# Kernel tuning notes

Hardware: AMD Instinct MI355X
Metric: run time of the kernel (lower is better)

## Reference

```python
import jax, jax.numpy as jnp
import numpy as np

N, N2, N3 = 40000, 20000, 10000
E, E2, E3 = 640000, 320000, 160000
HEADS = 4
F_IN = 5


def _glorot(k, shape):
    lim = float(np.sqrt(6.0 / (shape[0] + shape[-1])))
    return jax.random.uniform(k, shape, jnp.float32, -lim, lim)


def setup_inputs() -> dict:
    key = jax.random.key(0)
    ks = jax.random.split(key, 40)
    inp = {}
    inp["x"] = jax.random.normal(ks[0], (N, F_IN), jnp.float32)
    inp["edge_index"] = jax.random.randint(ks[1], (2, E), 0, N)
    inp["edge_index2"] = jax.random.randint(ks[2], (2, E2), 0, N2)
    inp["edge_index3"] = jax.random.randint(ks[3], (2, E3), 0, N3)
    # graclus-style cluster maps; constructed surjective so no cluster is empty
    inp["cluster1"] = jax.random.permutation(ks[4], jnp.arange(N) % N2)
    inp["cluster2"] = jax.random.permutation(ks[5], jnp.arange(N2) % N3)
    dims = [(F_IN, 16), (16, 32), (32, 64), (64, 32), (64, 16)]
    i = 6
    for idx, (fi, fo) in enumerate(dims, 1):
        inp[f"cW{idx}"] = _glorot(ks[i], (fi, HEADS * fo)); i += 1
        inp[f"cU{idx}"] = _glorot(ks[i], (fi, HEADS)); i += 1
        inp[f"cc{idx}"] = jnp.zeros((HEADS,), jnp.float32)
        inp[f"cb{idx}"] = jnp.zeros((fo,), jnp.float32)
    inp["l1W"] = _glorot(ks[i], (32, 256)); i += 1
    inp["l1b"] = jnp.zeros((256,), jnp.float32)
    inp["l2W"] = _glorot(ks[i], (256, 6890)); i += 1
    inp["l2b"] = jnp.zeros((6890,), jnp.float32)
    inp["oW"] = _glorot(ks[i], (6890, 1)); i += 1
    inp["ob"] = jnp.zeros((1,), jnp.float32)
    return inp


def feast_conv(x, ei, W, U, c, b, n, fo):
    """PyG FeaStConv: self-loops, per-edge head-softmax attention, mean aggregation."""
    sl = jnp.arange(n)
    src = jnp.concatenate([ei[0], sl])  # message sources (x_j)
    dst = jnp.concatenate([ei[1], sl])  # aggregation targets (x_i)
    xs, xd = x[src], x[dst]
    q = jax.nn.softmax((xs - xd) @ U + c, axis=-1)          # [E+n, H]
    m = (xs @ W).reshape(-1, HEADS, fo)                      # [E+n, H, fo]
    msg = jnp.einsum('eh,eho->eo', q, m)                     # [E+n, fo]
    agg = jax.ops.segment_sum(msg, dst, num_segments=n)
    cnt = jax.ops.segment_sum(jnp.ones((dst.shape[0],), x.dtype), dst, num_segments=n)
    return agg / cnt[:, None] + b


def _forward(x, edge_index, edge_index2, edge_index3, cluster1, cluster2, p):
    x1 = jax.nn.relu(feast_conv(x, edge_index, p["cW1"], p["cU1"], p["cc1"], p["cb1"], N, 16))
    x2 = jax.ops.segment_max(x1, cluster1, num_segments=N2)                     # graclus max_pool
    x2 = jax.nn.relu(feast_conv(x2, edge_index2, p["cW2"], p["cU2"], p["cc2"], p["cb2"], N2, 32))
    x3 = jax.ops.segment_max(x2, cluster2, num_segments=N3)
    x3 = jax.nn.relu(feast_conv(x3, edge_index3, p["cW3"], p["cU3"], p["cc3"], p["cb3"], N3, 64))
    x3 = jax.nn.relu(feast_conv(x3, edge_index3, p["cW4"], p["cU4"], p["cc4"], p["cb4"], N3, 32))
    x3 = jnp.concatenate([x2, x3[cluster2]], axis=1)                            # [N2, 64] unpool+skip
    x3 = jax.nn.relu(feast_conv(x3, edge_index2, p["cW5"], p["cU5"], p["cc5"], p["cb5"], N2, 16))
    h = jnp.concatenate([x1, x3[cluster1]], axis=1)                             # [N, 32]
    h = jax.nn.relu(h @ p["l1W"] + p["l1b"])
    h = jax.nn.relu(h @ p["l2W"] + p["l2b"])                                   # [N, 6890]
    return jax.nn.sigmoid(h @ p["oW"] + p["ob"])                                # [N, 1]


def reference(x, edge_index, edge_index2, edge_index3, cluster1, cluster2,
              cW1, cU1, cc1, cb1, cW2, cU2, cc2, cb2, cW3, cU3, cc3, cb3,
              cW4, cU4, cc4, cb4, cW5, cU5, cc5, cb5, l1W, l1b, l2W, l2b, oW, ob):
    p = dict(cW1=cW1, cU1=cU1, cc1=cc1, cb1=cb1, cW2=cW2, cU2=cU2, cc2=cc2, cb2=cb2,
             cW3=cW3, cU3=cU3, cc3=cc3, cb3=cb3, cW4=cW4, cU4=cU4, cc4=cc4, cb4=cb4,
             cW5=cW5, cU5=cU5, cc5=cc5, cb5=cb5, l1W=l1W, l1b=l1b, l2W=l2W, l2b=l2b,
             oW=oW, ob=ob)
    return _forward(x, edge_index, edge_index2, edge_index3, cluster1, cluster2, p)
```

## Files before the change

### kernel.cpp

```cpp
#include <hip/hip_runtime.h>
#include <math.h>

#define N1  40000
#define NN2 20000
#define NN3 10000
#define EE1 640000
#define EE2 320000
#define EE3 160000
#define ET  (EE1 + EE2 + EE3)
#define JPAD 6912
#define JREAL 6890
#define NTILE 432
#define CSPLIT 8
#define TPB (NTILE/CSPLIT)
#define NSTG (TPB/2)
#define NROWP 40192
#define NGRP 628
#define CAP 64

typedef __attribute__((ext_vector_type(8))) short short8;
typedef __attribute__((ext_vector_type(4))) float f32x4;

__device__ inline unsigned short f2bf(float f) {
  unsigned u = __float_as_uint(f);
  u += 0x7FFF + ((u >> 16) & 1);
  return (unsigned short)(u >> 16);
}

__device__ inline f32x4 qsoft(f32x4 xs, f32x4 xd, float c0, float c1, float c2, float c3) {
  float l0 = xs[0] - xd[0] + c0, l1 = xs[1] - xd[1] + c1;
  float l2 = xs[2] - xd[2] + c2, l3 = xs[3] - xd[3] + c3;
  float mx = fmaxf(fmaxf(l0, l1), fmaxf(l2, l3));
  float q0 = __expf(l0 - mx), q1 = __expf(l1 - mx);
  float q2 = __expf(l2 - mx), q3 = __expf(l3 - mx);
  float iv = 1.f / (q0 + q1 + q2 + q3);
  return (f32x4){q0 * iv, q1 * iv, q2 * iv, q3 * iv};
}

__global__ void k_matmulWU(const float* __restrict__ Xa, int fa,
                           const float* __restrict__ Xb, int fb,
                           const int* __restrict__ map,
                           const float* __restrict__ W, const float* __restrict__ U,
                           float* __restrict__ xW, float* __restrict__ xU,
                           int n, int co) {
  int ct = co + 4;
  int idx = blockIdx.x * 256 + threadIdx.x;
  if (idx >= n * ct) return;
  int row = idx / ct, col = idx - row * ct;
  const float* M;
  int stride;
  if (col < co) { M = W + col; stride = co; }
  else          { M = U + (col - co); stride = 4; }
  float s = 0.f;
  const float* ar = Xa + (size_t)row * fa;
  for (int k = 0; k < fa; ++k) s = fmaf(ar[k], M[(size_t)k * stride], s);
  if (Xb) {
    const float* br = Xb + (size_t)map[row] * fb;
    for (int k = 0; k < fb; ++k) s = fmaf(br[k], M[(size_t)(fa + k) * stride], s);
  }
  if (col < co) xW[(size_t)row * co + col] = s;
  else          xU[(size_t)row * 4 + (col - co)] = s;
}

__global__ void k_xU(const float* __restrict__ xin, const float* __restrict__ U,
                     float* __restrict__ xu, int n, int ci) {
  int idx = blockIdx.x * 256 + threadIdx.x;
  if (idx >= n * 4) return;
  int h = idx & 3, d = idx >> 2;
  const float* xr = xin + (size_t)d * ci;
  float s = 0.f;
  for (int k = 0; k < ci; ++k) s = fmaf(xr[k], U[k * 4 + h], s);
  xu[idx] = s;
}

__global__ void k_prep(const int* __restrict__ ei1, const int* __restrict__ ei2,
                       const int* __restrict__ ei3,
                       int* __restrict__ c1, int* __restrict__ c2, int* __restrict__ c3,
                       int* __restrict__ s1, int* __restrict__ s2, int* __restrict__ s3,
                       const float* __restrict__ x, float* __restrict__ x8,
                       const float* __restrict__ U1, float* __restrict__ xu1) {
  int i = blockIdx.x * 256 + threadIdx.x;
  if (i < ET) {
    int e = i;
    const int* ei; int* cnt; int* sl; int E;
    if (e < EE1) { ei = ei1; cnt = c1; sl = s1; E = EE1; }
    else {
      e -= EE1;
      if (e < EE2) { ei = ei2; cnt = c2; sl = s2; E = EE2; }
      else { e -= EE2; ei = ei3; cnt = c3; sl = s3; E = EE3; }
    }
    int s = ei[e], d = ei[E + e];
    int pos = atomicAdd(&cnt[d], 1);
    if (pos < CAP) sl[(size_t)d * CAP + pos] = s;
    return;
  }
  i -= ET;
  if (i < N1 * 8) {
    int d = i >> 3, k = i & 7;
    x8[i] = (k < 5) ? x[d * 5 + k] : 0.f;
    return;
  }
  i -= N1 * 8;
  if (i < N1 * 4) {
    int h = i & 3, d = i >> 2;
    const float* xr = x + (size_t)d * 5;
    float s = 0.f;
#pragma unroll
    for (int k = 0; k < 5; ++k) s = fmaf(xr[k], U1[k * 4 + h], s);
    xu1[i] = s;
  }
}

template<int CI4, int FO, int KREAL>
__global__ __launch_bounds__(256) void k_aggf(
    const int* __restrict__ cnt, const int* __restrict__ slots,
    const float* __restrict__ xU, const f32x4* __restrict__ xin4, int stride4,
    const float* __restrict__ c, const float* __restrict__ W,
    const float* __restrict__ b, float* __restrict__ outp, int n,
    const int* __restrict__ pool_cl, int* __restrict__ pool_out) {
  constexpr int LPN = CI4 * 4;
  constexpr int NB  = 256 / LPN;
  __shared__ float sh[NB][CI4 * 16];
  const int tid = threadIdx.x;
  const int nl = tid / LPN, li = tid - nl * LPN;
  const int cg = li >> 2, sp = li & 3;
  const int d = blockIdx.x * NB + nl;
  const float c0 = c[0], c1 = c[1], c2 = c[2], c3 = c[3];
  const f32x4* XU4 = (const f32x4*)xU;

  if (d < n) {
    const f32x4 xd = XU4[d];
    const int deg = min(cnt[d], CAP);
    const int jlo = (deg * sp) >> 2, jhi = (deg * (sp + 1)) >> 2;
    const int* sl = slots + (size_t)d * CAP;
    f32x4 acc[4];
#pragma unroll
    for (int e = 0; e < 4; ++e) acc[e] = (f32x4){0.f, 0.f, 0.f, 0.f};
    int j = jlo;
    for (; j + 4 <= jhi; j += 4) {
      int s0 = sl[j], s1 = sl[j + 1], s2 = sl[j + 2], s3 = sl[j + 3];
      f32x4 u0 = XU4[s0], u1 = XU4[s1], u2 = XU4[s2], u3 = XU4[s3];
      f32x4 v0 = xin4[(size_t)s0 * stride4 + cg];
      f32x4 v1 = xin4[(size_t)s1 * stride4 + cg];
      f32x4 v2 = xin4[(size_t)s2 * stride4 + cg];
      f32x4 v3 = xin4[(size_t)s3 * stride4 + cg];
      f32x4 q0 = qsoft(u0, xd, c0, c1, c2, c3);
      f32x4 q1 = qsoft(u1, xd, c0, c1, c2, c3);
      f32x4 q2 = qsoft(u2, xd, c0, c1, c2, c3);
      f32x4 q3 = qsoft(u3, xd, c0, c1, c2, c3);
#pragma unroll
      for (int e = 0; e < 4; ++e)
        acc[e] += v0[e] * q0 + v1[e] * q1 + v2[e] * q2 + v3[e] * q3;
    }
    for (; j < jhi; ++j) {
      int s = sl[j];
      f32x4 u = XU4[s];
      f32x4 v = xin4[(size_t)s * stride4 + cg];
      f32x4 q = qsoft(u, xd, c0, c1, c2, c3);
#pragma unroll
      for (int e = 0; e < 4; ++e) acc[e] += v[e] * q;
    }
#pragma unroll
    for (int e = 0; e < 4; ++e)
#pragma unroll
      for (int h = 0; h < 4; ++h) {
        acc[e][h] += __shfl_xor(acc[e][h], 1);
        acc[e][h] += __shfl_xor(acc[e][h], 2);
      }
    if (sp == 0) {
      float mx = fmaxf(fmaxf(c0, c1), fmaxf(c2, c3));
      float q0 = __expf(c0 - mx), q1 = __expf(c1 - mx);
      float q2 = __expf(c2 - mx), q3 = __expf(c3 - mx);
      float iv = 1.f / (q0 + q1 + q2 + q3);
      f32x4 q = (f32x4){q0 * iv, q1 * iv, q2 * iv, q3 * iv};
      f32x4 xv = xin4[(size_t)d * stride4 + cg];
#pragma unroll
      for (int e = 0; e < 4; ++e) {
        f32x4 a = acc[e] + xv[e] * q;
#pragma unroll
        for (int h = 0; h < 4; ++h) sh[nl][(cg * 4 + e) * 4 + h] = a[h];
      }
    }
  }
  __syncthreads();

  constexpr int NBFO = NB * FO;
#pragma unroll
  for (int base = 0; base < NBFO; base += 256) {
    int i2 = base + tid;
    if (i2 < NBFO) {
      int ln = i2 / FO, o = i2 - ln * FO;
      int d2 = blockIdx.x * NB + ln;
      if (d2 < n) {
        float acc2 = 0.f;
        const float* shl = sh[ln];
        for (int k = 0; k < KREAL; ++k) {
          const float* wr = W + (size_t)k * (4 * FO) + o;
          acc2 += shl[k * 4 + 0] * wr[0] + shl[k * 4 + 1] * wr[FO]
                + shl[k * 4 + 2] * wr[2 * FO] + shl[k * 4 + 3] * wr[3 * FO];
        }
        int deg2 = min(cnt[d2], CAP);
        float v = fmaxf(acc2 / (float)(deg2 + 1) + b[o], 0.f);
        outp[(size_t)d2 * FO + o] = v;
        if (pool_cl)
          atomicMax((int*)&pool_out[(size_t)pool_cl[d2] * FO + o], __float_as_int(v));
      }
    }
  }
}

__global__ void k_attagg4(const int* __restrict__ cnt, const int* __restrict__ slots,
                          const float* __restrict__ xU, const float4* __restrict__ xW,
                          const float* __restrict__ c, const float4* __restrict__ b4,
                          float4* __restrict__ outp, int n, int fo4,
                          const int* __restrict__ pool_cl, int* __restrict__ pool_out) {
  int idx = blockIdx.x * 256 + threadIdx.x;
  if (idx >= n * fo4 * 4) return;
  const int sp = idx & 3;
  const int t = idx >> 2;
  const int d = t / fo4, og = t - d * fo4;
  const float c0 = c[0], c1 = c[1], c2 = c[2], c3 = c[3];
  const float4 xd = *(const float4*)&xU[(size_t)d * 4];
  const int deg = min(cnt[d], CAP);
  const int jlo = (deg * sp) >> 2;
  const int jhi = (deg * (sp + 1)) >> 2;
  const int* sl = slots + (size_t)d * CAP;
  float ax = 0.f, ay = 0.f, az = 0.f, aw = 0.f;
  int j = jlo;
  for (; j + 2 <= jhi; j += 2) {
    int sA = sl[j], sB = sl[j + 1];
    float4 xsA = *(const float4*)&xU[(size_t)sA * 4];
    float4 xsB = *(const float4*)&xU[(size_t)sB * 4];
    const float4* mA = xW + (size_t)sA * 4 * fo4 + og;
    const float4* mB = xW + (size_t)sB * 4 * fo4 + og;
    float4 a0 = mA[0], a1 = mA[fo4], a2 = mA[2 * fo4], a3 = mA[3 * fo4];
    float4 e0 = mB[0], e1 = mB[fo4], e2 = mB[2 * fo4], e3 = mB[3 * fo4];
    float lA0 = xsA.x - xd.x + c0, lA1 = xsA.y - xd.y + c1;
    float lA2 = xsA.z - xd.z + c2, lA3 = xsA.w - xd.w + c3;
    float mxA = fmaxf(fmaxf(lA0, lA1), fmaxf(lA2, lA3));
    float qA0 = __expf(lA0 - mxA), qA1 = __expf(lA1 - mxA);
    float qA2 = __expf(lA2 - mxA), qA3 = __expf(lA3 - mxA);
    float ivA = 1.f / (qA0 + qA1 + qA2 + qA3);
    qA0 *= ivA; qA1 *= ivA; qA2 *= ivA; qA3 *= ivA;
    float lB0 = xsB.x - xd.x + c0, lB1 = xsB.y - xd.y + c1;
    float lB2 = xsB.z - xd.z + c2, lB3 = xsB.w - xd.w + c3;
    float mxB = fmaxf(fmaxf(lB0, lB1), fmaxf(lB2, lB3));
    float qB0 = __expf(lB0 - mxB), qB1 = __expf(lB1 - mxB);
    float qB2 = __expf(lB2 - mxB), qB3 = __expf(lB3 - mxB);
    float ivB = 1.f / (qB0 + qB1 + qB2 + qB3);
    qB0 *= ivB; qB1 *= ivB; qB2 *= ivB; qB3 *= ivB;
    ax += qA0 * a0.x + qA1 * a1.x + qA2 * a2.x + qA3 * a3.x
        + qB0 * e0.x + qB1 * e1.x + qB2 * e2.x + qB3 * e3.x;
    ay += qA0 * a0.y + qA1 * a1.y + qA2 * a2.y + qA3 * a3.y
        + qB0 * e0.y + qB1 * e1.y + qB2 * e2.y + qB3 * e3.y;
    az += qA0 * a0.z + qA1 * a1.z + qA2 * a2.z + qA3 * a3.z
        + qB0 * e0.z + qB1 * e1.z + qB2 * e2.z + qB3 * e3.z;
    aw += qA0 * a0.w + qA1 * a1.w + qA2 * a2.w + qA3 * a3.w
        + qB0 * e0.w + qB1 * e1.w + qB2 * e2.w + qB3 * e3.w;
  }
  if (j < jhi) {
    int s = sl[j];
    float4 xs = *(const float4*)&xU[(size_t)s * 4];
    const float4* m = xW + (size_t)s * 4 * fo4 + og;
    float4 m0 = m[0], m1 = m[fo4], m2 = m[2 * fo4], m3 = m[3 * fo4];
    float l0 = xs.x - xd.x + c0, l1 = xs.y - xd.y + c1;
    float l2 = xs.z - xd.z + c2, l3 = xs.w - xd.w + c3;
    float mx = fmaxf(fmaxf(l0, l1), fmaxf(l2, l3));
    float q0 = __expf(l0 - mx), q1 = __expf(l1 - mx);
    float q2 = __expf(l2 - mx), q3 = __expf(l3 - mx);
    float inv = 1.f / (q0 + q1 + q2 + q3);
    q0 *= inv; q1 *= inv; q2 *= inv; q3 *= inv;
    ax += q0 * m0.x + q1 * m1.x + q2 * m2.x + q3 * m3.x;
    ay += q0 * m0.y + q1 * m1.y + q2 * m2.y + q3 * m3.y;
    az += q0 * m0.z + q1 * m1.z + q2 * m2.z + q3 * m3.z;
    aw += q0 * m0.w + q1 * m1.w + q2 * m2.w + q3 * m3.w;
  }
  ax += __shfl_xor(ax, 1); ay += __shfl_xor(ay, 1);
  az += __shfl_xor(az, 1); aw += __shfl_xor(aw, 1);
  ax += __shfl_xor(ax, 2); ay += __shfl_xor(ay, 2);
  az += __shfl_xor(az, 2); aw += __shfl_xor(aw, 2);
  if (sp) return;
  {
    float mx = fmaxf(fmaxf(c0, c1), fmaxf(c2, c3));
    float q0 = __expf(c0 - mx), q1 = __expf(c1 - mx);
    float q2 = __expf(c2 - mx), q3 = __expf(c3 - mx);
    float inv = 1.f / (q0 + q1 + q2 + q3);
    const float4* m = xW + (size_t)d * 4 * fo4 + og;
    float4 m0 = m[0], m1 = m[fo4], m2 = m[2 * fo4], m3 = m[3 * fo4];
    ax += (q0 * m0.x + q1 * m1.x + q2 * m2.x + q3 * m3.x) * inv;
    ay += (q0 * m0.y + q1 * m1.y + q2 * m2.y + q3 * m3.y) * inv;
    az += (q0 * m0.z + q1 * m1.z + q2 * m2.z + q3 * m3.z) * inv;
    aw += (q0 * m0.w + q1 * m1.w + q2 * m2.w + q3 * m3.w) * inv;
  }
  const float inv = 1.f / (float)(deg + 1);
  const float4 bb = b4[og];
  float4 v;
  v.x = fmaxf(ax * inv + bb.x, 0.f);
  v.y = fmaxf(ay * inv + bb.y, 0.f);
  v.z = fmaxf(az * inv + bb.z, 0.f);
  v.w = fmaxf(aw * inv + bb.w, 0.f);
  outp[(size_t)d * fo4 + og] = v;
  if (pool_cl) {
    int* po = pool_out + ((size_t)pool_cl[d] * fo4 + og) * 4;
    atomicMax(&po[0], __float_as_int(v.x));
    atomicMax(&po[1], __float_as_int(v.y));
    atomicMax(&po[2], __float_as_int(v.z));
    atomicMax(&po[3], __float_as_int(v.w));
  }
}

__global__ __launch_bounds__(256) void k_packB(
    const float* __restrict__ l2W, short8* __restrict__ Bp,
    const float* __restrict__ l2b, const float* __restrict__ oW,
    float* __restrict__ l2bp, float* __restrict__ oWp) {
  __shared__ float tile[32][65];
  const int bid = blockIdx.x, tid = threadIdx.x;
  if (bid < 27) {
    int j = bid * 256 + tid;
    l2bp[j] = (j < JREAL) ? l2b[j] : 0.f;
    oWp[j]  = (j < JREAL) ? oW[j]  : 0.f;
  }
  const int kg = bid / 108, jg = bid - kg * 108;
  const int k0 = kg * 32, j0 = jg * 64;
  const int kr = tid >> 6, jc = tid & 63;
  const int j = j0 + jc;
#pragma unroll
  for (int i = 0; i < 8; ++i) {
    int row = kr * 8 + i;
    tile[row][jc] = (j < JREAL) ? l2W[(size_t)(k0 + row) * JREAL + j] : 0.f;
  }
  __syncthreads();
  const int tt = tid >> 6, lane = tid & 63;
  short8 v;
#pragma unroll
  for (int i = 0; i < 8; ++i)
    v[i] = (short)f2bf(tile[((lane >> 4) << 3) + i][tt * 16 + (lane & 15)]);
  Bp[((size_t)(jg * 4 + tt) * 8 + kg) * 64 + lane] = v;
}

__global__ __launch_bounds__(256) void k_packh(
    const float* __restrict__ x1, const float* __restrict__ x5,
    const int* __restrict__ cl1, const float* __restrict__ l1W,
    const float* __restrict__ l1b, short8* __restrict__ Apack) {
  __shared__ float h1s[64][256];
  const int tid = threadIdx.x;
  const int row0 = blockIdx.x * 64;

  float wcol[32];
#pragma unroll
  for (int k = 0; k < 32; ++k) wcol[k] = l1W[k * 256 + tid];
  const float bt = l1b[tid];

  for (int r = 0; r < 64; ++r) {
    const int row = row0 + r;
    float s = bt;
    if (row < N1) {
      const float* a = x1 + (size_t)row * 16;
      const float* b = x5 + (size_t)cl1[row] * 16;
#pragma unroll
      for (int k = 0; k < 16; ++k) s = fmaf(a[k], wcol[k], s);
#pragma unroll
      for (int k = 0; k < 16; ++k) s = fmaf(b[k], wcol[16 + k], s);
    }
    h1s[r][tid ^ ((r & 7) << 3)] = fmaxf(s, 0.f);
  }
  __syncthreads();

#pragma unroll
  for (int j = 0; j < 8; ++j) {
    int s = j * 256 + tid;
    int l = s & 63, ks = (s >> 6) & 7, rb = s >> 9;
    int row = rb * 16 + (l & 15);
    int col0 = (ks * 32 + ((l >> 4) << 3)) ^ ((row & 7) << 3);
    const float* sp = &h1s[row][col0];
    short8 v;
#pragma unroll
    for (int i = 0; i < 8; ++i) v[i] = (short)f2bf(sp[i]);
    Apack[(size_t)blockIdx.x * 2048 + s] = v;
  }
}

__global__ __launch_bounds__(256, 2) void k_final2(
    const short8* __restrict__ Apack, const short8* __restrict__ Bp,
    const float* __restrict__ l2bp, const float* __restrict__ oWp,
    float* __restrict__ zbuf) {
  __shared__ short8 bufs[2][1024];
  const int tid = threadIdx.x, wid = tid >> 6, l = tid & 63;
  const int rg = blockIdx.x >> 3, cg = blockIdx.x & 7;
  const int lm = l & 15, lh = l >> 4;

  short8 af[4][8];
  {
    const short8* ap = Apack + (size_t)(rg * 4 + wid) * 2048 + l;
#pragma unroll
    for (int rb = 0; rb < 4; ++rb)
#pragma unroll
      for (int ks = 0; ks < 8; ++ks) af[rb][ks] = ap[rb * 512 + ks * 64];
  }

  const short8* bsrc = Bp + (size_t)cg * TPB * 512;
  short8 n0 = bsrc[tid], n1 = bsrc[256 + tid], n2 = bsrc[512 + tid], n3 = bsrc[768 + tid];
  bufs[0][tid] = n0; bufs[0][256 + tid] = n1;
  bufs[0][512 + tid] = n2; bufs[0][768 + tid] = n3;
  {
    const short8* p = bsrc + 1024;
    n0 = p[tid]; n1 = p[256 + tid]; n2 = p[512 + tid]; n3 = p[768 + tid];
  }
  asm volatile("s_waitcnt lgkmcnt(0)" ::: "memory");
  __builtin_amdgcn_s_barrier();
  asm volatile("" ::: "memory");

  float zp[4][4];
#pragma unroll
  for (int rb = 0; rb < 4; ++rb)
#pragma unroll
    for (int r = 0; r < 4; ++r) zp[rb][r] = 0.f;

  for (int st = 0; st < NSTG; ++st) {
    const int cur = st & 1;
    if (st + 1 < NSTG) {
      bufs[cur ^ 1][tid] = n0; bufs[cur ^ 1][256 + tid] = n1;
      bufs[cur ^ 1][512 + tid] = n2; bufs[cur ^ 1][768 + tid] = n3;
    }
    if (st + 2 < NSTG) {
      const short8* p = bsrc + (st + 2) * 1024;
      n0 = p[tid]; n1 = p[256 + tid]; n2 = p[512 + tid]; n3 = p[768 + tid];
    }
#pragma unroll
    for (int half = 0; half < 2; ++half) {
      short8 bfr[8];
#pragma unroll
      for (int ks = 0; ks < 8; ++ks) bfr[ks] = bufs[cur][half * 512 + ks * 64 + l];

      f32x4 acc[4];
#pragma unroll
      for (int rb = 0; rb < 4; ++rb) acc[rb] = (f32x4){0.f, 0.f, 0.f, 0.f};
      __builtin_amdgcn_s_setprio(1);
#pragma unroll
      for (int ks = 0; ks < 8; ++ks)
#pragma unroll
        for (int rb = 0; rb < 4; ++rb)
          acc[rb] = __builtin_amdgcn_mfma_f32_16x16x32_bf16(af[rb][ks], bfr[ks], acc[rb], 0, 0, 0);
      __builtin_amdgcn_s_setprio(0);

      const int j = (cg * TPB + st * 2 + half) * 16 + lm;
      const float lb = l2bp[j];
      const float ow = oWp[j];
#pragma unroll
      for (int rb = 0; rb < 4; ++rb)
#pragma unroll
        for (int r = 0; r < 4; ++r)
          zp[rb][r] += fmaxf(acc[rb][r] + lb, 0.f) * ow;
    }
    asm volatile("s_waitcnt lgkmcnt(0)" ::: "memory");
    __builtin_amdgcn_s_barrier();
    asm volatile("" ::: "memory");
  }

#pragma unroll
  for (int m = 1; m < 16; m <<= 1)
#pragma unroll
    for (int rb = 0; rb < 4; ++rb)
#pragma unroll
      for (int r = 0; r < 4; ++r)
        zp[rb][r] += __shfl_xor(zp[rb][r], m);

  if (lm == 0) {
    const int rbase = rg * 256 + wid * 64 + lh * 4;
#pragma unroll
    for (int rb = 0; rb < 4; ++rb)
#pragma unroll
      for (int r = 0; r < 4; ++r)
        atomicAdd(&zbuf[rbase + rb * 16 + r], zp[rb][r]);
  }
}

__global__ void k_sigm(const float* __restrict__ zbuf, const float* __restrict__ ob,
                       float* __restrict__ out) {
  int i = blockIdx.x * 256 + threadIdx.x;
  if (i >= N1) return;
  out[i] = 1.f / (1.f + expf(-(zbuf[i] + ob[0])));
}

static void run_conv(const float* xa, int fa, const float* xb, int fb, const int* gmap,
                     const int* cnt, const int* slots, int n, int fo,
                     const float* W, const float* U, const float* c, const float* b,
                     float* outp, float* xW, float* xU,
                     const int* pool_cl, int* pool_out, hipStream_t stream) {
  int co = 4 * fo;
  k_matmulWU<<<(n * (co + 4) + 255) / 256, 256, 0, stream>>>(xa, fa, xb, fb, gmap,
                                                             W, U, xW, xU, n, co);
  k_attagg4<<<(n * (fo / 4) * 4 + 255) / 256, 256, 0, stream>>>(
      cnt, slots, xU, (const float4*)xW, c, (const float4*)b, (float4*)outp, n, fo / 4,
      pool_cl, pool_out);
}

extern "C" void kernel_launch(void* const* d_in, const int* in_sizes, int n_in,
                              void* d_out, int out_size, void* d_ws, size_t ws_size,
                              hipStream_t stream) {
  const float* x   = (const float*)d_in[0];
  const int* ei1   = (const int*)d_in[1];
  const int* ei2   = (const int*)d_in[2];
  const int* ei3   = (const int*)d_in[3];
  const int* cl1   = (const int*)d_in[4];
  const int* cl2   = (const int*)d_in[5];
  const float* cW1 = (const float*)d_in[6],  *cU1 = (const float*)d_in[7],
             * cc1 = (const float*)d_in[8],  *cb1 = (const float*)d_in[9];
  const float* cW2 = (const float*)d_in[10], *cU2 = (const float*)d_in[11],
             * cc2 = (const float*)d_in[12], *cb2 = (const float*)d_in[13];
  const float* cW3 = (const float*)d_in[14], *cU3 = (const float*)d_in[15],
             * cc3 = (const float*)d_in[16], *cb3 = (const float*)d_in[17];
  const float* cW4 = (const float*)d_in[18], *cU4 = (const float*)d_in[19],
             * cc4 = (const float*)d_in[20], *cb4 = (const float*)d_in[21];
  const float* cW5 = (const float*)d_in[22], *cU5 = (const float*)d_in[23],
             * cc5 = (const float*)d_in[24], *cb5 = (const float*)d_in[25];
  const float* l1W = (const float*)d_in[26], *l1b = (const float*)d_in[27];
  const float* l2W = (const float*)d_in[28], *l2b = (const float*)d_in[29];
  const float* oW  = (const float*)d_in[30], *ob  = (const float*)d_in[31];

  float* ws = (float*)d_ws;
  float* x2p  = ws + 0;
  float* x3p  = ws + 320000;
  float* zbuf = ws + 640000;
  int*  cnt1  = (int*)(ws + 680192);
  int*  cnt2  = (int*)(ws + 720192);
  int*  cnt3  = (int*)(ws + 740192);
  int*  sl1   = (int*)(ws + 750192);
  int*  sl2   = (int*)(ws + 3310192);
  int*  sl3   = (int*)(ws + 4590192);
  float* x3a  = ws + 5230192;
  float* x3b  = ws + 5870192;
  float* x1   = ws + 6190192;
  float* x2   = ws + 6830192;
  float* x5   = ws + 7470192;
  short8* Bp  = (short8*)(ws + 7790192);
  float* l2bp = ws + 8674928;
  float* oWp  = ws + 8681840;
  float* xW   = ws + 8688752;
  float* xu   = ws + 11248752;
  float* x8   = ws + 11408752;
  short8* Apack = (short8*)(ws + 750192);

  hipMemsetAsync(ws, 0, 750192 * sizeof(float), stream);
  k_packB<<<864, 256, 0, stream>>>(l2W, Bp, l2b, oW, l2bp, oWp);

  k_prep<<<(ET + N1 * 8 + N1 * 4 + 255) / 256, 256, 0, stream>>>(
      ei1, ei2, ei3, cnt1, cnt2, cnt3, sl1, sl2, sl3, x, x8, cU1, xu);

  k_aggf<2, 16, 5><<<(N1 + 31) / 32, 256, 0, stream>>>(
      cnt1, sl1, xu, (const f32x4*)x8, 2, cc1, cW1, cb1, x1, N1, cl1, (int*)x2p);
  k_xU<<<(NN2 * 4 + 255) / 256, 256, 0, stream>>>(x2p, cU2, xu, NN2, 16);
  k_aggf<4, 32, 16><<<(NN2 + 15) / 16, 256, 0, stream>>>(
      cnt2, sl2, xu, (const f32x4*)x2p, 4, cc2, cW2, cb2, x2, NN2, cl2, (int*)x3p);
  k_xU<<<(NN3 * 4 + 255) / 256, 256, 0, stream>>>(x3p, cU3, xu, NN3, 32);
  k_aggf<8, 64, 32><<<(NN3 + 7) / 8, 256, 0, stream>>>(
      cnt3, sl3, xu, (const f32x4*)x3p, 8, cc3, cW3, cb3, x3a, NN3, nullptr, nullptr);
  k_xU<<<(NN3 * 4 + 255) / 256, 256, 0, stream>>>(x3a, cU4, xu, NN3, 64);
  k_aggf<16, 32, 64><<<(NN3 + 3) / 4, 256, 0, stream>>>(
      cnt3, sl3, xu, (const f32x4*)x3a, 16, cc4, cW4, cb4, x3b, NN3, nullptr, nullptr);
  run_conv(x2, 32, x3b, 32, cl2, cnt2, sl2, NN2, 16,
           cW5, cU5, cc5, cb5, x5, xW, xu, nullptr, nullptr, stream);

  k_packh<<<NGRP, 256, 0, stream>>>(x1, x5, cl1, l1W, l1b, Apack);
  k_final2<<<(NROWP / 256) * CSPLIT, 256, 0, stream>>>(Apack, Bp, l2bp, oWp, zbuf);
  k_sigm<<<(N1 + 255) / 256, 256, 0, stream>>>(zbuf, ob, (float*)d_out);
}
```

Before: 426.3 us.

## Merge weight packing into prep kernel, fuse next-layer xU, use 16-bit slots

The l2W bf16 packing kernel is merged into the edge-bucketing prep kernel as extra blocks, which saves one launch and lets the two independent jobs run concurrently. Layer 3's aggregation kernel now computes the next layer's x@U projection from shared memory, removing a separate k_xU launch. Neighbor slot arrays are stored as 16-bit indices to halve slot traffic, which assumes node ids fit in 16 bits. With N1=40000 ids below 65536 this holds, but the code would break for larger graphs.

```diff
diff --git a/kernel.cpp b/kernel.cpp
--- a/kernel.cpp
+++ b/kernel.cpp
@@ -17,9 +17,11 @@
 #define NROWP 40192
 #define NGRP 628
 #define CAP 64
+#define PBK 864
 
 typedef __attribute__((ext_vector_type(8))) short short8;
 typedef __attribute__((ext_vector_type(4))) float f32x4;
+typedef unsigned short u16;
 
 __device__ inline unsigned short f2bf(float f) {
   unsigned u = __float_as_uint(f);
@@ -73,16 +75,46 @@
   xu[idx] = s;
 }
 
-__global__ void k_prep(const int* __restrict__ ei1, const int* __restrict__ ei2,
-                       const int* __restrict__ ei3,
-                       int* __restrict__ c1, int* __restrict__ c2, int* __restrict__ c3,
-                       int* __restrict__ s1, int* __restrict__ s2, int* __restrict__ s3,
-                       const float* __restrict__ x, float* __restrict__ x8,
-                       const float* __restrict__ U1, float* __restrict__ xu1) {
-  int i = blockIdx.x * 256 + threadIdx.x;
+__global__ __launch_bounds__(256) void k_setup(
+    const float* __restrict__ l2W, short8* __restrict__ Bp,
+    const float* __restrict__ l2b, const float* __restrict__ oW,
+    float* __restrict__ l2bp, float* __restrict__ oWp,
+    const int* __restrict__ ei1, const int* __restrict__ ei2,
+    const int* __restrict__ ei3,
+    int* __restrict__ c1, int* __restrict__ c2, int* __restrict__ c3,
+    u16* __restrict__ s1, u16* __restrict__ s2, u16* __restrict__ s3,
+    const float* __restrict__ x, float* __restrict__ x8,
+    const float* __restrict__ U1, float* __restrict__ xu1) {
+  __shared__ float tile[32][65];
+  const int bid = blockIdx.x, tid = threadIdx.x;
+  if (bid < PBK) {
+    if (bid < 27) {
+      int j = bid * 256 + tid;
+      l2bp[j] = (j < JREAL) ? l2b[j] : 0.f;
+      oWp[j]  = (j < JREAL) ? oW[j]  : 0.f;
+    }
+    const int kg = bid / 108, jg = bid - kg * 108;
+    const int k0 = kg * 32, j0 = jg * 64;
+    const int kr = tid >> 6, jc = tid & 63;
+    const int j = j0 + jc;
+#pragma unroll
+    for (int i = 0; i < 8; ++i) {
+      int row = kr * 8 + i;
+      tile[row][jc] = (j < JREAL) ? l2W[(size_t)(k0 + row) * JREAL + j] : 0.f;
+    }
+    __syncthreads();
+    const int tt = tid >> 6, lane = tid & 63;
+    short8 v;
+#pragma unroll
+    for (int i = 0; i < 8; ++i)
+      v[i] = (short)f2bf(tile[((lane >> 4) << 3) + i][tt * 16 + (lane & 15)]);
+    Bp[((size_t)(jg * 4 + tt) * 8 + kg) * 64 + lane] = v;
+    return;
+  }
+  int i = (bid - PBK) * 256 + tid;
   if (i < ET) {
     int e = i;
-    const int* ei; int* cnt; int* sl; int E;
+    const int* ei; int* cnt; u16* sl; int E;
     if (e < EE1) { ei = ei1; cnt = c1; sl = s1; E = EE1; }
     else {
       e -= EE1;
@@ -91,7 +123,7 @@
     }
     int s = ei[e], d = ei[E + e];
     int pos = atomicAdd(&cnt[d], 1);
-    if (pos < CAP) sl[(size_t)d * CAP + pos] = s;
+    if (pos < CAP) sl[(size_t)d * CAP + pos] = (u16)s;
     return;
   }
   i -= ET;
@@ -111,16 +143,18 @@
   }
 }
 
-template<int CI4, int FO, int KREAL>
+template<int CI4, int FO, int KREAL, bool XUOUT>
 __global__ __launch_bounds__(256) void k_aggf(
-    const int* __restrict__ cnt, const int* __restrict__ slots,
+    const int* __restrict__ cnt, const u16* __restrict__ slots,
     const float* __restrict__ xU, const f32x4* __restrict__ xin4, int stride4,
     const float* __restrict__ c, const float* __restrict__ W,
     const float* __restrict__ b, float* __restrict__ outp, int n,
-    const int* __restrict__ pool_cl, int* __restrict__ pool_out) {
+    const int* __restrict__ pool_cl, int* __restrict__ pool_out,
+    const float* __restrict__ Unext, float* __restrict__ xunext) {
   constexpr int LPN = CI4 * 4;
   constexpr int NB  = 256 / LPN;
   __shared__ float sh[NB][CI4 * 16];
+  __shared__ float sh2[NB][FO];
   const int tid = threadIdx.x;
   const int nl = tid / LPN, li = tid - nl * LPN;
   const int cg = li >> 2, sp = li & 3;
@@ -132,7 +166,7 @@
     const f32x4 xd = XU4[d];
     const int deg = min(cnt[d], CAP);
     const int jlo = (deg * sp) >> 2, jhi = (deg * (sp + 1)) >> 2;
-    const int* sl = slots + (size_t)d * CAP;
+    const u16* sl = slots + (size_t)d * CAP;
     f32x4 acc[4];
 #pragma unroll
     for (int e = 0; e < 4; ++e) acc[e] = (f32x4){0.f, 0.f, 0.f, 0.f};
@@ -202,14 +236,29 @@
         int deg2 = min(cnt[d2], CAP);
         float v = fmaxf(acc2 / (float)(deg2 + 1) + b[o], 0.f);
         outp[(size_t)d2 * FO + o] = v;
+        if (XUOUT) sh2[ln][o] = v;
         if (pool_cl)
           atomicMax((int*)&pool_out[(size_t)pool_cl[d2] * FO + o], __float_as_int(v));
       }
     }
   }
-}
-
-__global__ void k_attagg4(const int* __restrict__ cnt, const int* __restrict__ slots,
+
+  if (XUOUT) {
+    __syncthreads();
+    if (tid < NB * 4) {
+      int ln = tid >> 2, h = tid & 3;
+      int d3 = blockIdx.x * NB + ln;
+      if (d3 < n) {
+        float s = 0.f;
+        const float* so = sh2[ln];
+        for (int o = 0; o < FO; ++o) s = fmaf(so[o], Unext[o * 4 + h], s);
+        xunext[(size_t)d3 * 4 + h] = s;
+      }
+    }
+  }
+}
+
+__global__ void k_attagg4(const int* __restrict__ cnt, const u16* __restrict__ slots,
                           const float* __restrict__ xU, const float4* __restrict__ xW,
                           const float* __restrict__ c, const float4* __restrict__ b4,
                           float4* __restrict__ outp, int n, int fo4,
@@ -224,7 +273,7 @@
   const int deg = min(cnt[d], CAP);
   const int jlo = (deg * sp) >> 2;
   const int jhi = (deg * (sp + 1)) >> 2;
-  const int* sl = slots + (size_t)d * CAP;
+  const u16* sl = slots + (size_t)d * CAP;
   float ax = 0.f, ay = 0.f, az = 0.f, aw = 0.f;
   int j = jlo;
   for (; j + 2 <= jhi; j += 2) {
@@ -309,35 +358,6 @@
   }
 }
 
-__global__ __launch_bounds__(256) void k_packB(
-    const float* __restrict__ l2W, short8* __restrict__ Bp,
-    const float* __restrict__ l2b, const float* __restrict__ oW,
-    float* __restrict__ l2bp, float* __restrict__ oWp) {
-  __shared__ float tile[32][65];
-  const int bid = blockIdx.x, tid = threadIdx.x;
-  if (bid < 27) {
-    int j = bid * 256 + tid;
-    l2bp[j] = (j < JREAL) ? l2b[j] : 0.f;
-    oWp[j]  = (j < JREAL) ? oW[j]  : 0.f;
-  }
-  const int kg = bid / 108, jg = bid - kg * 108;
-  const int k0 = kg * 32, j0 = jg * 64;
-  const int kr = tid >> 6, jc = tid & 63;
-  const int j = j0 + jc;
-#pragma unroll
-  for (int i = 0; i < 8; ++i) {
-    int row = kr * 8 + i;
-    tile[row][jc] = (j < JREAL) ? l2W[(size_t)(k0 + row) * JREAL + j] : 0.f;
-  }
-  __syncthreads();
-  const int tt = tid >> 6, lane = tid & 63;
-  short8 v;
-#pragma unroll
-  for (int i = 0; i < 8; ++i)
-    v[i] = (short)f2bf(tile[((lane >> 4) << 3) + i][tt * 16 + (lane & 15)]);
-  Bp[((size_t)(jg * 4 + tt) * 8 + kg) * 64 + lane] = v;
-}
-
 __global__ __launch_bounds__(256) void k_packh(
     const float* __restrict__ x1, const float* __restrict__ x5,
     const int* __restrict__ cl1, const float* __restrict__ l1W,
@@ -480,19 +500,6 @@
   int i = blockIdx.x * 256 + threadIdx.x;
   if (i >= N1) return;
   out[i] = 1.f / (1.f + expf(-(zbuf[i] + ob[0])));
-}
-
-static void run_conv(const float* xa, int fa, const float* xb, int fb, const int* gmap,
-                     const int* cnt, const int* slots, int n, int fo,
-                     const float* W, const float* U, const float* c, const float* b,
-                     float* outp, float* xW, float* xU,
-                     const int* pool_cl, int* pool_out, hipStream_t stream) {
-  int co = 4 * fo;
-  k_matmulWU<<<(n * (co + 4) + 255) / 256, 256, 0, stream>>>(xa, fa, xb, fb, gmap,
-                                                             W, U, xW, xU, n, co);
-  k_attagg4<<<(n * (fo / 4) * 4 + 255) / 256, 256, 0, stream>>>(
-      cnt, slots, xU, (const float4*)xW, c, (const float4*)b, (float4*)outp, n, fo / 4,
-      pool_cl, pool_out);
 }
 
 extern "C" void kernel_launch(void* const* d_in, const int* in_sizes, int n_in,
@@ -525,41 +532,49 @@
   int*  cnt1  = (int*)(ws + 680192);
   int*  cnt2  = (int*)(ws + 720192);
   int*  cnt3  = (int*)(ws + 740192);
-  int*  sl1   = (int*)(ws + 750192);
-  int*  sl2   = (int*)(ws + 3310192);
-  int*  sl3   = (int*)(ws + 4590192);
-  float* x3a  = ws + 5230192;
-  float* x3b  = ws + 5870192;
-  float* x1   = ws + 6190192;
-  float* x2   = ws + 6830192;
-  float* x5   = ws + 7470192;
-  short8* Bp  = (short8*)(ws + 7790192);
-  float* l2bp = ws + 8674928;
-  float* oWp  = ws + 8681840;
-  float* xW   = ws + 8688752;
-  float* xu   = ws + 11248752;
-  float* x8   = ws + 11408752;
-  short8* Apack = (short8*)(ws + 750192);
+  float* x1   = ws + 750192;
+  float* x2   = ws + 1390192;
+  float* x5   = ws + 2030192;
+  short8* Bp  = (short8*)(ws + 2350192);
+  float* l2bp = ws + 3234928;
+  float* oWp  = ws + 3241840;
+  u16*  sl1   = (u16*)(ws + 3248752);
+  u16*  sl2   = (u16*)(ws + 4528752);
+  u16*  sl3   = (u16*)(ws + 5168752);
+  float* x3a  = ws + 5488752;
+  float* x3b  = ws + 6128752;
+  float* x8   = ws + 6448752;
+  float* xu   = ws + 6768752;
+  float* xub  = ws + 6928752;
+  float* xW   = ws + 6968752;
+  short8* Apack = (short8*)(ws + 3248752);
 
   hipMemsetAsync(ws, 0, 750192 * sizeof(float), stream);
-  k_packB<<<864, 256, 0, stream>>>(l2W, Bp, l2b, oW, l2bp, oWp);
-
-  k_prep<<<(ET + N1 * 8 + N1 * 4 + 255) / 256, 256, 0, stream>>>(
+
+  const int prepThreads = ET + N1 * 8 + N1 * 4;
+  k_setup<<<PBK + (prepThreads + 255) / 256, 256, 0, stream>>>(
+      l2W, Bp, l2b, oW, l2bp, oWp,
       ei1, ei2, ei3, cnt1, cnt2, cnt3, sl1, sl2, sl3, x, x8, cU1, xu);
 
-  k_aggf<2, 16, 5><<<(N1 + 31) / 32, 256, 0, stream>>>(
-      cnt1, sl1, xu, (const f32x4*)x8, 2, cc1, cW1, cb1, x1, N1, cl1, (int*)x2p);
+  k_aggf<2, 16, 5, false><<<(N1 + 31) / 32, 256, 0, stream>>>(
+      cnt1, sl1, xu, (const f32x4*)x8, 2, cc1, cW1, cb1, x1, N1, cl1, (int*)x2p,
+      nullptr, nullptr);
   k_xU<<<(NN2 * 4 + 255) / 256, 256, 0, stream>>>(x2p, cU2, xu, NN2, 16);
-  k_aggf<4, 32, 16><<<(NN2 + 15) / 16, 256, 0, stream>>>(
-      cnt2, sl2, xu, (const f32x4*)x2p, 4, cc2, cW2, cb2, x2, NN2, cl2, (int*)x3p);
+  k_aggf<4, 32, 16, false><<<(NN2 + 15) / 16, 256, 0, stream>>>(
+      cnt2, sl2, xu, (const f32x4*)x2p, 4, cc2, cW2, cb2, x2, NN2, cl2, (int*)x3p,
+      nullptr, nullptr);
   k_xU<<<(NN3 * 4 + 255) / 256, 256, 0, stream>>>(x3p, cU3, xu, NN3, 32);
-  k_aggf<8, 64, 32><<<(NN3 + 7) / 8, 256, 0, stream>>>(
-      cnt3, sl3, xu, (const f32x4*)x3p, 8, cc3, cW3, cb3, x3a, NN3, nullptr, nullptr);
-  k_xU<<<(NN3 * 4 + 255) / 256, 256, 0, stream>>>(x3a, cU4, xu, NN3, 64);
-  k_aggf<16, 32, 64><<<(NN3 + 3) / 4, 256, 0, stream>>>(
-      cnt3, sl3, xu, (const f32x4*)x3a, 16, cc4, cW4, cb4, x3b, NN3, nullptr, nullptr);
-  run_conv(x2, 32, x3b, 32, cl2, cnt2, sl2, NN2, 16,
-           cW5, cU5, cc5, cb5, x5, xW, xu, nullptr, nullptr, stream);
+  k_aggf<8, 64, 32, true><<<(NN3 + 7) / 8, 256, 0, stream>>>(
+      cnt3, sl3, xu, (const f32x4*)x3p, 8, cc3, cW3, cb3, x3a, NN3, nullptr, nullptr,
+      cU4, xub);
+  k_aggf<16, 32, 64, false><<<(NN3 + 3) / 4, 256, 0, stream>>>(
+      cnt3, sl3, xub, (const f32x4*)x3a, 16, cc4, cW4, cb4, x3b, NN3, nullptr, nullptr,
+      nullptr, nullptr);
+  k_matmulWU<<<(NN2 * 68 + 255) / 256, 256, 0, stream>>>(x2, 32, x3b, 32, cl2,
+                                                         cW5, cU5, xW, xu, NN2, 64);
+  k_attagg4<<<(NN2 * 4 * 4 + 255) / 256, 256, 0, stream>>>(
+      cnt2, sl2, xu, (const float4*)xW, cc5, (const float4*)cb5, (float4*)x5, NN2, 4,
+      nullptr, nullptr);
 
   k_packh<<<NGRP, 256, 0, stream>>>(x1, x5, cl1, l1W, l1b, Apack);
   k_final2<<<(NROWP / 256) * CSPLIT, 256, 0, stream>>>(Apack, Bp, l2bp, oWp, zbuf);
```

Measured after the change: 410.6 us. 3.7% less time.
